# Kernel tuning notes

Measured on AMD Instinct MI355X. Metric: run time of the kernel, lower is better.

## Reference

```python
import jax, jax.numpy as jnp
import numpy as np

B, T, S, DIN, H = 64, 512, 4, 64, 128  # slices S, per-slice input DIN, per-slice hidden H
HTOT = S * H  # 512


def setup_inputs() -> dict:
    key = jax.random.key(0)
    ks = jax.random.split(key, 6)
    stdv = 1.0 / np.sqrt(HTOT)
    u = lambda k, shape: jax.random.uniform(k, shape, jnp.float32, -stdv, stdv)
    x = jax.random.normal(ks[0], (B, T, S * DIN), jnp.float32)
    Ws = u(ks[1], (S, DIN, 4 * H))      # stacked per-slice input weights
    Us = u(ks[2], (S, H, 4 * H))        # stacked per-slice recurrent weights
    biases = u(ks[3], (S, 4 * H))       # stacked per-slice biases
    Wc = u(ks[4], (HTOT, 4 * HTOT))     # connector weights
    bc = u(ks[5], (4 * HTOT,))          # connector biases
    return {"x": x, "Ws": Ws, "Us": Us, "biases": biases, "Wc": Wc, "bc": bc}


def reference(x, Ws, Us, biases, Wc, bc):
    b, t, _ = x.shape
    xt = jnp.swapaxes(x.reshape(b, t, S, DIN), 0, 1)  # (T, B, S, DIN)
    h0 = jnp.zeros((b, HTOT), x.dtype)
    c0 = jnp.zeros((b, HTOT), x.dtype)

    def step(carry, x_t):
        h, c = carry
        hs = h.reshape(b, S, H)
        # block-diagonal per-slice gates: (B, S, 4H)
        gates = (jnp.einsum('bsi,sio->bso', x_t, Ws)
                 + jnp.einsum('bsh,sho->bso', hs, Us)
                 + biases)
        i1 = jax.nn.sigmoid(gates[..., :H]).reshape(b, HTOT)
        f1 = jax.nn.sigmoid(gates[..., H:2 * H]).reshape(b, HTOT)
        g1 = jnp.tanh(gates[..., 2 * H:3 * H]).reshape(b, HTOT)
        o1 = jax.nn.sigmoid(gates[..., 3 * H:]).reshape(b, HTOT)
        # connector stage
        i_t = jax.nn.sigmoid(i1 @ Wc[:, :HTOT] + bc[:HTOT])
        f_t = jax.nn.sigmoid(f1 @ Wc[:, HTOT:2 * HTOT] + bc[HTOT:2 * HTOT])
        g_t = jnp.tanh(g1 @ Wc[:, 2 * HTOT:3 * HTOT] + bc[2 * HTOT:3 * HTOT])
        o_t = jax.nn.sigmoid(o1 @ Wc[:, 3 * HTOT:] + bc[3 * HTOT:])
        c_new = f_t * c + i_t * g_t
        h_new = o_t * jnp.tanh(c_new)
        return (h_new, c_new), h_new

    (h_t, c_t), hseq = jax.lax.scan(step, (h0, c0), xt)
    hidden_seq = jnp.swapaxes(hseq, 0, 1)  # (B, T, HTOT)
    return hidden_seq, h_t, c_t
```

## Files before the change

kernel.cpp:

```cpp
#include <hip/hip_runtime.h>
#include <hip/hip_bf16.h>


typedef unsigned short u16;
typedef unsigned long long u64;
typedef __attribute__((ext_vector_type(8))) short short8;
typedef __attribute__((ext_vector_type(4))) float floatx4;

#define NT 256
#define NBLK 128
#define TSTEPS 512

#define WS_FLAG1 0
#define WS_FLAG2 1024
#define WS_H_HI 2048
#define WS_ZERO_BYTES (WS_H_HI + 65536)
#define WS_ACT_HI (WS_ZERO_BYTES)
#define ACT_PLANE 131072

__device__ __forceinline__ float b2f(u16 u) {
  unsigned v = ((unsigned)u) << 16;
  float f;
  __builtin_memcpy(&f, &v, 4);
  return f;
}
__device__ __forceinline__ u16 f2b(float f) {
  __hip_bfloat16 h = __float2bfloat16(f);
  u16 u;
  __builtin_memcpy(&u, &h, 2);
  return u;
}
__device__ __forceinline__ float sigf(float x) { return 1.0f / (1.0f + __expf(-x)); }
__device__ __forceinline__ float tanhf_fast(float x) { return 2.0f * sigf(2.0f * x) - 1.0f; }
__device__ __forceinline__ short8 ld8(const u16* p) { return *(const short8*)p; }

__device__ __forceinline__ short8 lda_frag(const u16* p) {
  union {
    u64 q[2];
    short8 s;
  } u;
  u.q[0] = __hip_atomic_load((const u64*)p, __ATOMIC_RELAXED, __HIP_MEMORY_SCOPE_AGENT);
  u.q[1] = __hip_atomic_load((const u64*)(p + 4), __ATOMIC_RELAXED, __HIP_MEMORY_SCOPE_AGENT);
  return u.s;
}
__device__ __forceinline__ void sta16(u16* p, u16 v) {
  __hip_atomic_store(p, v, __ATOMIC_RELAXED, __HIP_MEMORY_SCOPE_AGENT);
}

__device__ __forceinline__ void split8v(float4 a, float4 b, short8& hi, short8& lo) {
  float v[8] = {a.x, a.y, a.z, a.w, b.x, b.y, b.z, b.w};
#pragma unroll
  for (int i = 0; i < 8; ++i) {
    u16 h = f2b(v[i]);
    hi[i] = (short)h;
    lo[i] = (short)f2b(v[i] - b2f(h));
  }
}

__device__ __forceinline__ void wait_flags(unsigned* flags, int nmask, unsigned target) {
  if (threadIdx.x < 64) {
    const int fi = threadIdx.x & nmask;
    int spins = 0;
    for (;;) {
      const unsigned v =
          __hip_atomic_load(&flags[fi], __ATOMIC_RELAXED, __HIP_MEMORY_SCOPE_AGENT);
      if (__ballot(v >= target) == ~0ULL) break;
      if (++spins > (1 << 24)) break;
      __builtin_amdgcn_s_sleep(1);
    }
  }
  __syncthreads();
}
__device__ __forceinline__ void arrive_flags(unsigned* flags, int myidx, unsigned target) {
  asm volatile("s_waitcnt vmcnt(0)" ::: "memory");
  __syncthreads();
  if (threadIdx.x == 0)
    __hip_atomic_store(&flags[myidx], target, __ATOMIC_RELAXED, __HIP_MEMORY_SCOPE_AGENT);
}

__global__ void __launch_bounds__(NT) init_ws_kernel(unsigned* w, int n) {
  int i = blockIdx.x * blockDim.x + threadIdx.x;
  const int st = gridDim.x * blockDim.x;
  for (; i < n; i += st) w[i] = 0u;
}

__global__ void __launch_bounds__(NT, 1) slicelstm_kernel(
    const float* __restrict__ x, const float* __restrict__ Ws,
    const float* __restrict__ Us, const float* __restrict__ biases,
    const float* __restrict__ Wc, const float* __restrict__ bcg,
    float* __restrict__ out, u16* __restrict__ act_hi, u16* __restrict__ h_hi,
    unsigned* __restrict__ flagbase) {
  __shared__ __align__(16) u16 W1H[64 * 200];
  __shared__ __align__(16) u16 W2H[64 * 520];
  __shared__ float gx[4][16][17];

  const int tid = threadIdx.x;
  const int blk = blockIdx.x;
  const int q = blk & 3;
  const int jt = blk >> 2;
  const int j0 = jt * 16;
  const int s = j0 >> 7;
  const int jbase = j0 & 127;
  unsigned* flags1 = flagbase + q * 64;
  unsigned* flags2 = flagbase + 256 + (q * 4 + s) * 16;

  for (int i = tid; i < 64 * 192; i += NT) {
    const int r = i / 192, k = i % 192;
    const int col = (r >> 4) * 128 + jbase + (r & 15);
    const float w = (k < 64) ? Ws[(size_t)(s * 64 + k) * 512 + col]
                             : Us[(size_t)(s * 128 + (k - 64)) * 512 + col];
    W1H[r * 200 + k] = f2b(w);
  }
  for (int i = tid; i < 64 * 512; i += NT) {
    const int r = i >> 9, k = i & 511;
    const int col = (r >> 4) * 512 + j0 + (r & 15);
    W2H[r * 520 + k] = f2b(Wc[(size_t)k * 2048 + col]);
  }

  const int lane = tid & 63;
  const int g = tid >> 6;
  const int lm = lane & 15;
  const int lq = lane >> 4;
  const int ko = lq * 8;

  short8 w1l[6], w2l[16];
#pragma unroll
  for (int kt = 0; kt < 6; ++kt) {
    const int col = (g << 7) + jbase + lm;
#pragma unroll
    for (int e = 0; e < 8; ++e) {
      const int k = kt * 32 + ko + e;
      const float w = (k < 64) ? Ws[(size_t)(s * 64 + k) * 512 + col]
                               : Us[(size_t)(s * 128 + (k - 64)) * 512 + col];
      w1l[kt][e] = (short)f2b(w - b2f(f2b(w)));
    }
  }
#pragma unroll
  for (int kt = 0; kt < 16; ++kt) {
    const int col = (g << 9) + j0 + lm;
#pragma unroll
    for (int e = 0; e < 8; ++e) {
      const float w = Wc[(size_t)(kt * 32 + ko + e) * 2048 + col];
      w2l[kt][e] = (short)f2b(w - b2f(f2b(w)));
    }
  }
  const float biasv = biases[s * 512 + (g << 7) + jbase + lm];
  const float bcv = bcg[(g << 9) + j0 + lm];
  __syncthreads();

  const u16* w1r = &W1H[((g << 4) + lm) * 200];
  const u16* w2r = &W2H[((g << 4) + lm) * 520];
  const int brow = q * 16 + lm;
  const float* xrow = x + (size_t)brow * (512 * 256) + s * 64;
  const int hbase = brow * 512 + s * 128;
  const int arow_off = ((g << 6) + brow) * 512;

  const int p3b = tid >> 4, p3j = tid & 15;
  const int p3ci = (q * 16 + p3b) * 512 + j0 + p3j;
  const size_t obase = (size_t)(q * 16 + p3b) * TSTEPS * 512 + j0 + p3j;
  float creg = 0.f, hprev = 0.f;

  float4 xa0, xb0, xa1, xb1;
  {
    const float* xp = xrow;
    xa0 = *(const float4*)(xp + ko);
    xb0 = *(const float4*)(xp + ko + 4);
    xa1 = *(const float4*)(xp + 32 + ko);
    xb1 = *(const float4*)(xp + 32 + ko + 4);
  }

  for (int t = 0; t < TSTEPS; ++t) {
    short8 xh[2], xl[2];
    split8v(xa0, xb0, xh[0], xl[0]);
    split8v(xa1, xb1, xh[1], xl[1]);
    floatx4 accA = {0.f, 0.f, 0.f, 0.f}, accB = {0.f, 0.f, 0.f, 0.f};
    floatx4 accC = {0.f, 0.f, 0.f, 0.f};
#pragma unroll
    for (int kt = 0; kt < 2; ++kt) {
      const short8 bh = ld8(w1r + kt * 32 + ko);
      accA = __builtin_amdgcn_mfma_f32_16x16x32_bf16(xh[kt], bh, accA, 0, 0, 0);
      accB = __builtin_amdgcn_mfma_f32_16x16x32_bf16(xl[kt], bh, accB, 0, 0, 0);
      accC = __builtin_amdgcn_mfma_f32_16x16x32_bf16(xh[kt], w1l[kt], accC, 0, 0, 0);
    }

    wait_flags(flags2, 7, (unsigned)t);

    short8 hh[4];
#pragma unroll
    for (int kt = 0; kt < 4; ++kt) hh[kt] = lda_frag(&h_hi[hbase + kt * 32 + ko]);
    asm volatile("s_waitcnt vmcnt(0)" ::: "memory");
    __builtin_amdgcn_sched_barrier(0);

    {
#pragma unroll
      for (int kt = 0; kt < 4; ++kt) {
        const short8 bh = ld8(w1r + 64 + kt * 32 + ko);
        accA = __builtin_amdgcn_mfma_f32_16x16x32_bf16(hh[kt], bh, accA, 0, 0, 0);
        accC = __builtin_amdgcn_mfma_f32_16x16x32_bf16(hh[kt], w1l[2 + kt], accC, 0, 0, 0);
      }
      const int pp = (t & 1) * ACT_PLANE;
#pragma unroll
      for (int r = 0; r < 4; ++r) {
        const int b = q * 16 + lq * 4 + r;
        const float pre = accA[r] + accB[r] + accC[r] + biasv;
        const float a = (g == 2) ? tanhf_fast(pre) : sigf(pre);
        sta16(&act_hi[pp + ((g << 6) + b) * 512 + j0 + lm], f2b(a));
      }
    }
    arrive_flags(flags1, jt, (unsigned)(t + 1));
    if (t > 0) __builtin_nontemporal_store(hprev, &out[obase + (size_t)(t - 1) * 512]);
    {
      const float* xp = xrow + (size_t)(t < TSTEPS - 1 ? (t + 1) : t) * 256;
      xa0 = *(const float4*)(xp + ko);
      xb0 = *(const float4*)(xp + ko + 4);
      xa1 = *(const float4*)(xp + 32 + ko);
      xb1 = *(const float4*)(xp + 32 + ko + 4);
    }
    __builtin_amdgcn_sched_barrier(0);
    wait_flags(flags1, 31, (unsigned)(t + 1));

    short8 Ah[16];
    {
      const u16* ahp = act_hi + (t & 1) * ACT_PLANE + arow_off;
#pragma unroll
      for (int kt = 0; kt < 16; ++kt) Ah[kt] = lda_frag(ahp + kt * 32 + ko);
    }
    asm volatile("s_waitcnt vmcnt(0)" ::: "memory");
    __builtin_amdgcn_sched_barrier(0);
    floatx4 a2a = {0.f, 0.f, 0.f, 0.f}, a2b = {0.f, 0.f, 0.f, 0.f};
    floatx4 a2c = {0.f, 0.f, 0.f, 0.f}, a2d = {0.f, 0.f, 0.f, 0.f};
#pragma unroll
    for (int kt = 0; kt < 16; kt += 2) {
      const int kb0 = kt * 32 + ko, kb1 = kb0 + 32;
      const short8 Bh0 = ld8(w2r + kb0), Bh1 = ld8(w2r + kb1);
      a2a = __builtin_amdgcn_mfma_f32_16x16x32_bf16(Ah[kt], Bh0, a2a, 0, 0, 0);
      a2b = __builtin_amdgcn_mfma_f32_16x16x32_bf16(Ah[kt], w2l[kt], a2b, 0, 0, 0);
      a2c = __builtin_amdgcn_mfma_f32_16x16x32_bf16(Ah[kt + 1], Bh1, a2c, 0, 0, 0);
      a2d = __builtin_amdgcn_mfma_f32_16x16x32_bf16(Ah[kt + 1], w2l[kt + 1], a2d, 0, 0, 0);
    }
#pragma unroll
    for (int r = 0; r < 4; ++r)
      gx[g][lq * 4 + r][lm] = (a2a[r] + a2c[r]) + (a2b[r] + a2d[r]) + bcv;
    __syncthreads();

    {
      const float it = sigf(gx[0][p3b][p3j]);
      const float ft = sigf(gx[1][p3b][p3j]);
      const float gt = tanhf_fast(gx[2][p3b][p3j]);
      const float ot = sigf(gx[3][p3b][p3j]);
      const float cn = ft * creg + it * gt;
      creg = cn;
      const float h = ot * tanhf_fast(cn);
      hprev = h;
      if (t < TSTEPS - 1) {
        sta16(&h_hi[p3ci], f2b(h));
      } else {
        __builtin_nontemporal_store(h, &out[obase + (size_t)t * 512]);
        __builtin_nontemporal_store(h, &out[16777216 + p3ci]);
        __builtin_nontemporal_store(cn, &out[16777216 + 32768 + p3ci]);
      }
    }
    if (t < TSTEPS - 1) arrive_flags(flags2, jt & 7, (unsigned)(t + 1));
  }
}

extern "C" void kernel_launch(void* const* d_in, const int* in_sizes, int n_in,
                              void* d_out, int out_size, void* d_ws, size_t ws_size,
                              hipStream_t stream) {
  const float* x = (const float*)d_in[0];
  const float* Ws = (const float*)d_in[1];
  const float* Us = (const float*)d_in[2];
  const float* biases = (const float*)d_in[3];
  const float* Wc = (const float*)d_in[4];
  const float* bc = (const float*)d_in[5];

  char* ws = (char*)d_ws;
  unsigned* flagbase = (unsigned*)(ws + WS_FLAG1);
  u16* h_hi = (u16*)(ws + WS_H_HI);
  u16* act_hi = (u16*)(ws + WS_ACT_HI);

  hipLaunchKernelGGL(init_ws_kernel, dim3(64), dim3(NT), 0, stream, (unsigned*)ws,
                     WS_ZERO_BYTES / 4);
  hipLaunchKernelGGL(slicelstm_kernel, dim3(NBLK), dim3(NT), 0, stream, x, Ws, Us,
                     biases, Wc, bc, (float*)d_out, act_hi, h_hi, flagbase);
}
```

Before: 4.442 ms.

## Replace flag barriers with per-element step tags packed beside bf16 data

Removes the separate flag arrays and the wait/arrive barrier protocol. Each bf16 value is now stored in a 32-bit word together with a step tag, and consumers spin-poll the data itself until every tag matches the expected step. The aim is to cut the store-drain, __syncthreads and flag round-trip latency on the critical path of each recurrent step. In exchange the activation and hidden-state traffic doubles, the workspace that must be zeroed grows, and a failed poll re-reads the whole fragment set.

```diff
diff --git a/kernel.cpp b/kernel.cpp
--- a/kernel.cpp
+++ b/kernel.cpp
@@ -11,12 +11,10 @@
 #define NBLK 128
 #define TSTEPS 512
 
-#define WS_FLAG1 0
-#define WS_FLAG2 1024
-#define WS_H_HI 2048
-#define WS_ZERO_BYTES (WS_H_HI + 65536)
-#define WS_ACT_HI (WS_ZERO_BYTES)
-#define ACT_PLANE 131072
+#define WS_H 0
+#define WS_ACT 131072
+#define ACT_PLANE_U32 131072
+#define WS_ZERO_BYTES (131072 + 2 * 524288)
 
 __device__ __forceinline__ float b2f(u16 u) {
   unsigned v = ((unsigned)u) << 16;
@@ -34,16 +32,10 @@
 __device__ __forceinline__ float tanhf_fast(float x) { return 2.0f * sigf(2.0f * x) - 1.0f; }
 __device__ __forceinline__ short8 ld8(const u16* p) { return *(const short8*)p; }
 
-__device__ __forceinline__ short8 lda_frag(const u16* p) {
-  union {
-    u64 q[2];
-    short8 s;
-  } u;
-  u.q[0] = __hip_atomic_load((const u64*)p, __ATOMIC_RELAXED, __HIP_MEMORY_SCOPE_AGENT);
-  u.q[1] = __hip_atomic_load((const u64*)(p + 4), __ATOMIC_RELAXED, __HIP_MEMORY_SCOPE_AGENT);
-  return u.s;
-}
-__device__ __forceinline__ void sta16(u16* p, u16 v) {
+__device__ __forceinline__ u64 ald64(const u64* p) {
+  return __hip_atomic_load(p, __ATOMIC_RELAXED, __HIP_MEMORY_SCOPE_AGENT);
+}
+__device__ __forceinline__ void ast32(unsigned* p, unsigned v) {
   __hip_atomic_store(p, v, __ATOMIC_RELAXED, __HIP_MEMORY_SCOPE_AGENT);
 }
 
@@ -57,26 +49,19 @@
   }
 }
 
-__device__ __forceinline__ void wait_flags(unsigned* flags, int nmask, unsigned target) {
-  if (threadIdx.x < 64) {
-    const int fi = threadIdx.x & nmask;
-    int spins = 0;
-    for (;;) {
-      const unsigned v =
-          __hip_atomic_load(&flags[fi], __ATOMIC_RELAXED, __HIP_MEMORY_SCOPE_AGENT);
-      if (__ballot(v >= target) == ~0ULL) break;
-      if (++spins > (1 << 24)) break;
-      __builtin_amdgcn_s_sleep(1);
-    }
-  }
-  __syncthreads();
-}
-__device__ __forceinline__ void arrive_flags(unsigned* flags, int myidx, unsigned target) {
-  asm volatile("s_waitcnt vmcnt(0)" ::: "memory");
-  __syncthreads();
-  if (threadIdx.x == 0)
-    __hip_atomic_store(&flags[myidx], target, __ATOMIC_RELAXED, __HIP_MEMORY_SCOPE_AGENT);
-}
+#define TAG_MASK 0x0000ffff0000ffffULL
+
+#define EXTRACT4(dst, d0, d1, d2, d3)              \
+  do {                                             \
+    dst[0] = (short)((d0) >> 16);                  \
+    dst[1] = (short)((d0) >> 48);                  \
+    dst[2] = (short)((d1) >> 16);                  \
+    dst[3] = (short)((d1) >> 48);                  \
+    dst[4] = (short)((d2) >> 16);                  \
+    dst[5] = (short)((d2) >> 48);                  \
+    dst[6] = (short)((d3) >> 16);                  \
+    dst[7] = (short)((d3) >> 48);                  \
+  } while (0)
 
 __global__ void __launch_bounds__(NT) init_ws_kernel(unsigned* w, int n) {
   int i = blockIdx.x * blockDim.x + threadIdx.x;
@@ -88,8 +73,8 @@
     const float* __restrict__ x, const float* __restrict__ Ws,
     const float* __restrict__ Us, const float* __restrict__ biases,
     const float* __restrict__ Wc, const float* __restrict__ bcg,
-    float* __restrict__ out, u16* __restrict__ act_hi, u16* __restrict__ h_hi,
-    unsigned* __restrict__ flagbase) {
+    float* __restrict__ out, unsigned* __restrict__ actbuf,
+    unsigned* __restrict__ hbuf) {
   __shared__ __align__(16) u16 W1H[64 * 200];
   __shared__ __align__(16) u16 W2H[64 * 520];
   __shared__ float gx[4][16][17];
@@ -101,8 +86,6 @@
   const int j0 = jt * 16;
   const int s = j0 >> 7;
   const int jbase = j0 & 127;
-  unsigned* flags1 = flagbase + q * 64;
-  unsigned* flags2 = flagbase + 256 + (q * 4 + s) * 16;
 
   for (int i = tid; i < 64 * 192; i += NT) {
     const int r = i / 192, k = i % 192;
@@ -183,13 +166,24 @@
       accC = __builtin_amdgcn_mfma_f32_16x16x32_bf16(xh[kt], w1l[kt], accC, 0, 0, 0);
     }
 
-    wait_flags(flags2, 7, (unsigned)t);
-
     short8 hh[4];
-#pragma unroll
-    for (int kt = 0; kt < 4; ++kt) hh[kt] = lda_frag(&h_hi[hbase + kt * 32 + ko]);
-    asm volatile("s_waitcnt vmcnt(0)" ::: "memory");
-    __builtin_amdgcn_sched_barrier(0);
+    {
+      const u64 tg2 = ((u64)(unsigned)t << 32) | (unsigned)t;
+      int tries = 0;
+      for (;;) {
+        u64 bad = 0;
+#pragma unroll
+        for (int kt = 0; kt < 4; ++kt) {
+          const u64* p = (const u64*)&hbuf[hbase + kt * 32 + ko];
+          const u64 d0 = ald64(p), d1 = ald64(p + 1);
+          const u64 d2 = ald64(p + 2), d3 = ald64(p + 3);
+          bad |= ((d0 ^ tg2) | (d1 ^ tg2) | (d2 ^ tg2) | (d3 ^ tg2)) & TAG_MASK;
+          EXTRACT4(hh[kt], d0, d1, d2, d3);
+        }
+        if (__ballot(bad == 0) == ~0ULL) break;
+        if (++tries > (1 << 12)) break;
+      }
+    }
 
     {
 #pragma unroll
@@ -198,16 +192,37 @@
         accA = __builtin_amdgcn_mfma_f32_16x16x32_bf16(hh[kt], bh, accA, 0, 0, 0);
         accC = __builtin_amdgcn_mfma_f32_16x16x32_bf16(hh[kt], w1l[2 + kt], accC, 0, 0, 0);
       }
-      const int pp = (t & 1) * ACT_PLANE;
+      const int pp = (t & 1) * ACT_PLANE_U32;
 #pragma unroll
       for (int r = 0; r < 4; ++r) {
         const int b = q * 16 + lq * 4 + r;
         const float pre = accA[r] + accB[r] + accC[r] + biasv;
         const float a = (g == 2) ? tanhf_fast(pre) : sigf(pre);
-        sta16(&act_hi[pp + ((g << 6) + b) * 512 + j0 + lm], f2b(a));
-      }
-    }
-    arrive_flags(flags1, jt, (unsigned)(t + 1));
+        ast32(&actbuf[pp + ((g << 6) + b) * 512 + j0 + lm],
+              ((unsigned)f2b(a) << 16) | (unsigned)(t + 1));
+      }
+    }
+
+    short8 Ah[16];
+    {
+      const unsigned* ap = actbuf + (t & 1) * ACT_PLANE_U32 + arow_off;
+      const u64 tg2 = ((u64)(unsigned)(t + 1) << 32) | (unsigned)(t + 1);
+      int tries = 0;
+      for (;;) {
+        u64 bad = 0;
+#pragma unroll
+        for (int kt = 0; kt < 16; ++kt) {
+          const u64* p = (const u64*)(ap + kt * 32 + ko);
+          const u64 d0 = ald64(p), d1 = ald64(p + 1);
+          const u64 d2 = ald64(p + 2), d3 = ald64(p + 3);
+          bad |= ((d0 ^ tg2) | (d1 ^ tg2) | (d2 ^ tg2) | (d3 ^ tg2)) & TAG_MASK;
+          EXTRACT4(Ah[kt], d0, d1, d2, d3);
+        }
+        if (__ballot(bad == 0) == ~0ULL) break;
+        if (++tries > (1 << 12)) break;
+      }
+    }
+
     if (t > 0) __builtin_nontemporal_store(hprev, &out[obase + (size_t)(t - 1) * 512]);
     {
       const float* xp = xrow + (size_t)(t < TSTEPS - 1 ? (t + 1) : t) * 256;
@@ -216,17 +231,7 @@
       xa1 = *(const float4*)(xp + 32 + ko);
       xb1 = *(const float4*)(xp + 32 + ko + 4);
     }
-    __builtin_amdgcn_sched_barrier(0);
-    wait_flags(flags1, 31, (unsigned)(t + 1));
-
-    short8 Ah[16];
-    {
-      const u16* ahp = act_hi + (t & 1) * ACT_PLANE + arow_off;
-#pragma unroll
-      for (int kt = 0; kt < 16; ++kt) Ah[kt] = lda_frag(ahp + kt * 32 + ko);
-    }
-    asm volatile("s_waitcnt vmcnt(0)" ::: "memory");
-    __builtin_amdgcn_sched_barrier(0);
+
     floatx4 a2a = {0.f, 0.f, 0.f, 0.f}, a2b = {0.f, 0.f, 0.f, 0.f};
     floatx4 a2c = {0.f, 0.f, 0.f, 0.f}, a2d = {0.f, 0.f, 0.f, 0.f};
 #pragma unroll
@@ -253,14 +258,14 @@
       const float h = ot * tanhf_fast(cn);
       hprev = h;
       if (t < TSTEPS - 1) {
-        sta16(&h_hi[p3ci], f2b(h));
+        ast32(&hbuf[p3ci], ((unsigned)f2b(h) << 16) | (unsigned)(t + 1));
       } else {
         __builtin_nontemporal_store(h, &out[obase + (size_t)t * 512]);
         __builtin_nontemporal_store(h, &out[16777216 + p3ci]);
         __builtin_nontemporal_store(cn, &out[16777216 + 32768 + p3ci]);
       }
     }
-    if (t < TSTEPS - 1) arrive_flags(flags2, jt & 7, (unsigned)(t + 1));
+    __syncthreads();
   }
 }
 
@@ -275,12 +280,11 @@
   const float* bc = (const float*)d_in[5];
 
   char* ws = (char*)d_ws;
-  unsigned* flagbase = (unsigned*)(ws + WS_FLAG1);
-  u16* h_hi = (u16*)(ws + WS_H_HI);
-  u16* act_hi = (u16*)(ws + WS_ACT_HI);
-
-  hipLaunchKernelGGL(init_ws_kernel, dim3(64), dim3(NT), 0, stream, (unsigned*)ws,
+  unsigned* hbuf = (unsigned*)(ws + WS_H);
+  unsigned* actbuf = (unsigned*)(ws + WS_ACT);
+
+  hipLaunchKernelGGL(init_ws_kernel, dim3(128), dim3(NT), 0, stream, (unsigned*)ws,
                      WS_ZERO_BYTES / 4);
   hipLaunchKernelGGL(slicelstm_kernel, dim3(NBLK), dim3(NT), 0, stream, x, Ws, Us,
-                     biases, Wc, bc, (float*)d_out, act_hi, h_hi, flagbase);
-}
+                     biases, Wc, bc, (float*)d_out, actbuf, hbuf);
+}
```

Result: slower. 9.617 ms (+116.5%).

## Halve grid and interleave two batch groups per block to overlap barrier waits

Applied to the files above, without the earlier changes.

Each block now handles two batch quarters (A and B) instead of one, so the grid shrinks from 128 to 64 blocks. The stage-1 and stage-2 work for the two groups is interleaved, so one group's computation can fill the time spent waiting on the other group's inter-block flags. This is meant to hide cross-block synchronisation latency on the sequential critical path. In exchange each block does twice the serial work per step and needs more registers, which may lengthen the per-step critical path.

```diff
diff --git a/kernel.cpp b/kernel.cpp
--- a/kernel.cpp
+++ b/kernel.cpp
@@ -8,7 +8,7 @@
 typedef __attribute__((ext_vector_type(4))) float floatx4;
 
 #define NT 256
-#define NBLK 128
+#define NBLK 64
 #define TSTEPS 512
 
 #define WS_FLAG1 0
@@ -92,17 +92,20 @@
     unsigned* __restrict__ flagbase) {
   __shared__ __align__(16) u16 W1H[64 * 200];
   __shared__ __align__(16) u16 W2H[64 * 520];
-  __shared__ float gx[4][16][17];
+  __shared__ float gx[2][4][16][17];
 
   const int tid = threadIdx.x;
   const int blk = blockIdx.x;
-  const int q = blk & 3;
-  const int jt = blk >> 2;
+  const int qA = blk & 1;
+  const int qB = qA + 2;
+  const int jt = blk >> 1;
   const int j0 = jt * 16;
   const int s = j0 >> 7;
   const int jbase = j0 & 127;
-  unsigned* flags1 = flagbase + q * 64;
-  unsigned* flags2 = flagbase + 256 + (q * 4 + s) * 16;
+  unsigned* flags1A = flagbase + qA * 64;
+  unsigned* flags1B = flagbase + qB * 64;
+  unsigned* flags2A = flagbase + 256 + (qA * 4 + s) * 16;
+  unsigned* flags2B = flagbase + 256 + (qB * 4 + s) * 16;
 
   for (int i = tid; i < 64 * 192; i += NT) {
     const int r = i / 192, k = i % 192;
@@ -150,117 +153,208 @@
 
   const u16* w1r = &W1H[((g << 4) + lm) * 200];
   const u16* w2r = &W2H[((g << 4) + lm) * 520];
-  const int brow = q * 16 + lm;
-  const float* xrow = x + (size_t)brow * (512 * 256) + s * 64;
-  const int hbase = brow * 512 + s * 128;
-  const int arow_off = ((g << 6) + brow) * 512;
+  const int browA = qA * 16 + lm;
+  const int browB = qB * 16 + lm;
+  const float* xrowA = x + (size_t)browA * (512 * 256) + s * 64;
+  const float* xrowB = x + (size_t)browB * (512 * 256) + s * 64;
+  const int hbaseA = browA * 512 + s * 128;
+  const int hbaseB = browB * 512 + s * 128;
+  const int arowA = ((g << 6) + browA) * 512;
+  const int arowB = ((g << 6) + browB) * 512;
 
   const int p3b = tid >> 4, p3j = tid & 15;
-  const int p3ci = (q * 16 + p3b) * 512 + j0 + p3j;
-  const size_t obase = (size_t)(q * 16 + p3b) * TSTEPS * 512 + j0 + p3j;
-  float creg = 0.f, hprev = 0.f;
-
-  float4 xa0, xb0, xa1, xb1;
+  const int p3ciA = (qA * 16 + p3b) * 512 + j0 + p3j;
+  const int p3ciB = (qB * 16 + p3b) * 512 + j0 + p3j;
+  const size_t obaseA = (size_t)(qA * 16 + p3b) * TSTEPS * 512 + j0 + p3j;
+  const size_t obaseB = (size_t)(qB * 16 + p3b) * TSTEPS * 512 + j0 + p3j;
+  float cregA = 0.f, hprevA = 0.f, cregB = 0.f, hprevB = 0.f;
+
+  float4 xa0A, xb0A, xa1A, xb1A, xa0B, xb0B, xa1B, xb1B;
   {
-    const float* xp = xrow;
-    xa0 = *(const float4*)(xp + ko);
-    xb0 = *(const float4*)(xp + ko + 4);
-    xa1 = *(const float4*)(xp + 32 + ko);
-    xb1 = *(const float4*)(xp + 32 + ko + 4);
+    const float* xp = xrowA;
+    xa0A = *(const float4*)(xp + ko);
+    xb0A = *(const float4*)(xp + ko + 4);
+    xa1A = *(const float4*)(xp + 32 + ko);
+    xb1A = *(const float4*)(xp + 32 + ko + 4);
+    const float* xq = xrowB;
+    xa0B = *(const float4*)(xq + ko);
+    xb0B = *(const float4*)(xq + ko + 4);
+    xa1B = *(const float4*)(xq + 32 + ko);
+    xb1B = *(const float4*)(xq + 32 + ko + 4);
   }
 
   for (int t = 0; t < TSTEPS; ++t) {
-    short8 xh[2], xl[2];
-    split8v(xa0, xb0, xh[0], xl[0]);
-    split8v(xa1, xb1, xh[1], xl[1]);
-    floatx4 accA = {0.f, 0.f, 0.f, 0.f}, accB = {0.f, 0.f, 0.f, 0.f};
-    floatx4 accC = {0.f, 0.f, 0.f, 0.f};
+    const int pp = (t & 1) * ACT_PLANE;
+    floatx4 aA = {0.f, 0.f, 0.f, 0.f}, aB = {0.f, 0.f, 0.f, 0.f};
+    floatx4 aC = {0.f, 0.f, 0.f, 0.f};
+    {
+      short8 xh[2], xl[2];
+      split8v(xa0A, xb0A, xh[0], xl[0]);
+      split8v(xa1A, xb1A, xh[1], xl[1]);
+#pragma unroll
+      for (int kt = 0; kt < 2; ++kt) {
+        const short8 bh = ld8(w1r + kt * 32 + ko);
+        aA = __builtin_amdgcn_mfma_f32_16x16x32_bf16(xh[kt], bh, aA, 0, 0, 0);
+        aB = __builtin_amdgcn_mfma_f32_16x16x32_bf16(xl[kt], bh, aB, 0, 0, 0);
+        aC = __builtin_amdgcn_mfma_f32_16x16x32_bf16(xh[kt], w1l[kt], aC, 0, 0, 0);
+      }
+      wait_flags(flags2A, 7, (unsigned)t);
+      short8 hh[4];
+#pragma unroll
+      for (int kt = 0; kt < 4; ++kt) hh[kt] = lda_frag(&h_hi[hbaseA + kt * 32 + ko]);
+      asm volatile("s_waitcnt vmcnt(0)" ::: "memory");
+      __builtin_amdgcn_sched_barrier(0);
+#pragma unroll
+      for (int kt = 0; kt < 4; ++kt) {
+        const short8 bh = ld8(w1r + 64 + kt * 32 + ko);
+        aA = __builtin_amdgcn_mfma_f32_16x16x32_bf16(hh[kt], bh, aA, 0, 0, 0);
+        aC = __builtin_amdgcn_mfma_f32_16x16x32_bf16(hh[kt], w1l[2 + kt], aC, 0, 0, 0);
+      }
+#pragma unroll
+      for (int r = 0; r < 4; ++r) {
+        const int b = qA * 16 + lq * 4 + r;
+        const float pre = aA[r] + aB[r] + aC[r] + biasv;
+        const float a = (g == 2) ? tanhf_fast(pre) : sigf(pre);
+        sta16(&act_hi[pp + ((g << 6) + b) * 512 + j0 + lm], f2b(a));
+      }
+    }
+    floatx4 bA = {0.f, 0.f, 0.f, 0.f}, bB = {0.f, 0.f, 0.f, 0.f};
+    floatx4 bC = {0.f, 0.f, 0.f, 0.f};
+    short8 xhB[2], xlB[2];
+    split8v(xa0B, xb0B, xhB[0], xlB[0]);
+    split8v(xa1B, xb1B, xhB[1], xlB[1]);
 #pragma unroll
     for (int kt = 0; kt < 2; ++kt) {
       const short8 bh = ld8(w1r + kt * 32 + ko);
-      accA = __builtin_amdgcn_mfma_f32_16x16x32_bf16(xh[kt], bh, accA, 0, 0, 0);
-      accB = __builtin_amdgcn_mfma_f32_16x16x32_bf16(xl[kt], bh, accB, 0, 0, 0);
-      accC = __builtin_amdgcn_mfma_f32_16x16x32_bf16(xh[kt], w1l[kt], accC, 0, 0, 0);
-    }
-
-    wait_flags(flags2, 7, (unsigned)t);
-
-    short8 hh[4];
-#pragma unroll
-    for (int kt = 0; kt < 4; ++kt) hh[kt] = lda_frag(&h_hi[hbase + kt * 32 + ko]);
-    asm volatile("s_waitcnt vmcnt(0)" ::: "memory");
-    __builtin_amdgcn_sched_barrier(0);
-
-    {
+      bA = __builtin_amdgcn_mfma_f32_16x16x32_bf16(xhB[kt], bh, bA, 0, 0, 0);
+      bB = __builtin_amdgcn_mfma_f32_16x16x32_bf16(xlB[kt], bh, bB, 0, 0, 0);
+      bC = __builtin_amdgcn_mfma_f32_16x16x32_bf16(xhB[kt], w1l[kt], bC, 0, 0, 0);
+    }
+    arrive_flags(flags1A, jt, (unsigned)(t + 1));
+    if (t > 0) __builtin_nontemporal_store(hprevA, &out[obaseA + (size_t)(t - 1) * 512]);
+    {
+      const float* xp = xrowA + (size_t)(t < TSTEPS - 1 ? (t + 1) : t) * 256;
+      xa0A = *(const float4*)(xp + ko);
+      xb0A = *(const float4*)(xp + ko + 4);
+      xa1A = *(const float4*)(xp + 32 + ko);
+      xb1A = *(const float4*)(xp + 32 + ko + 4);
+    }
+    {
+      wait_flags(flags2B, 7, (unsigned)t);
+      short8 hh[4];
+#pragma unroll
+      for (int kt = 0; kt < 4; ++kt) hh[kt] = lda_frag(&h_hi[hbaseB + kt * 32 + ko]);
+      asm volatile("s_waitcnt vmcnt(0)" ::: "memory");
+      __builtin_amdgcn_sched_barrier(0);
 #pragma unroll
       for (int kt = 0; kt < 4; ++kt) {
         const short8 bh = ld8(w1r + 64 + kt * 32 + ko);
-        accA = __builtin_amdgcn_mfma_f32_16x16x32_bf16(hh[kt], bh, accA, 0, 0, 0);
-        accC = __builtin_amdgcn_mfma_f32_16x16x32_bf16(hh[kt], w1l[2 + kt], accC, 0, 0, 0);
-      }
-      const int pp = (t & 1) * ACT_PLANE;
+        bA = __builtin_amdgcn_mfma_f32_16x16x32_bf16(hh[kt], bh, bA, 0, 0, 0);
+        bC = __builtin_amdgcn_mfma_f32_16x16x32_bf16(hh[kt], w1l[2 + kt], bC, 0, 0, 0);
+      }
 #pragma unroll
       for (int r = 0; r < 4; ++r) {
-        const int b = q * 16 + lq * 4 + r;
-        const float pre = accA[r] + accB[r] + accC[r] + biasv;
+        const int b = qB * 16 + lq * 4 + r;
+        const float pre = bA[r] + bB[r] + bC[r] + biasv;
         const float a = (g == 2) ? tanhf_fast(pre) : sigf(pre);
         sta16(&act_hi[pp + ((g << 6) + b) * 512 + j0 + lm], f2b(a));
       }
     }
-    arrive_flags(flags1, jt, (unsigned)(t + 1));
-    if (t > 0) __builtin_nontemporal_store(hprev, &out[obase + (size_t)(t - 1) * 512]);
-    {
-      const float* xp = xrow + (size_t)(t < TSTEPS - 1 ? (t + 1) : t) * 256;
-      xa0 = *(const float4*)(xp + ko);
-      xb0 = *(const float4*)(xp + ko + 4);
-      xa1 = *(const float4*)(xp + 32 + ko);
-      xb1 = *(const float4*)(xp + 32 + ko + 4);
-    }
-    __builtin_amdgcn_sched_barrier(0);
-    wait_flags(flags1, 31, (unsigned)(t + 1));
-
-    short8 Ah[16];
-    {
-      const u16* ahp = act_hi + (t & 1) * ACT_PLANE + arow_off;
+    arrive_flags(flags1B, jt, (unsigned)(t + 1));
+    if (t > 0) __builtin_nontemporal_store(hprevB, &out[obaseB + (size_t)(t - 1) * 512]);
+    {
+      const float* xp = xrowB + (size_t)(t < TSTEPS - 1 ? (t + 1) : t) * 256;
+      xa0B = *(const float4*)(xp + ko);
+      xb0B = *(const float4*)(xp + ko + 4);
+      xa1B = *(const float4*)(xp + 32 + ko);
+      xb1B = *(const float4*)(xp + 32 + ko + 4);
+    }
+
+    {
+      wait_flags(flags1A, 31, (unsigned)(t + 1));
+      short8 Ah[16];
+      const u16* ahp = act_hi + pp + arowA;
 #pragma unroll
       for (int kt = 0; kt < 16; ++kt) Ah[kt] = lda_frag(ahp + kt * 32 + ko);
-    }
-    asm volatile("s_waitcnt vmcnt(0)" ::: "memory");
-    __builtin_amdgcn_sched_barrier(0);
-    floatx4 a2a = {0.f, 0.f, 0.f, 0.f}, a2b = {0.f, 0.f, 0.f, 0.f};
-    floatx4 a2c = {0.f, 0.f, 0.f, 0.f}, a2d = {0.f, 0.f, 0.f, 0.f};
-#pragma unroll
-    for (int kt = 0; kt < 16; kt += 2) {
-      const int kb0 = kt * 32 + ko, kb1 = kb0 + 32;
-      const short8 Bh0 = ld8(w2r + kb0), Bh1 = ld8(w2r + kb1);
-      a2a = __builtin_amdgcn_mfma_f32_16x16x32_bf16(Ah[kt], Bh0, a2a, 0, 0, 0);
-      a2b = __builtin_amdgcn_mfma_f32_16x16x32_bf16(Ah[kt], w2l[kt], a2b, 0, 0, 0);
-      a2c = __builtin_amdgcn_mfma_f32_16x16x32_bf16(Ah[kt + 1], Bh1, a2c, 0, 0, 0);
-      a2d = __builtin_amdgcn_mfma_f32_16x16x32_bf16(Ah[kt + 1], w2l[kt + 1], a2d, 0, 0, 0);
-    }
-#pragma unroll
-    for (int r = 0; r < 4; ++r)
-      gx[g][lq * 4 + r][lm] = (a2a[r] + a2c[r]) + (a2b[r] + a2d[r]) + bcv;
+      asm volatile("s_waitcnt vmcnt(0)" ::: "memory");
+      __builtin_amdgcn_sched_barrier(0);
+      floatx4 c0 = {0.f, 0.f, 0.f, 0.f}, c1 = {0.f, 0.f, 0.f, 0.f};
+      floatx4 c2 = {0.f, 0.f, 0.f, 0.f}, c3 = {0.f, 0.f, 0.f, 0.f};
+#pragma unroll
+      for (int kt = 0; kt < 16; kt += 2) {
+        const int kb0 = kt * 32 + ko, kb1 = kb0 + 32;
+        const short8 Bh0 = ld8(w2r + kb0), Bh1 = ld8(w2r + kb1);
+        c0 = __builtin_amdgcn_mfma_f32_16x16x32_bf16(Ah[kt], Bh0, c0, 0, 0, 0);
+        c1 = __builtin_amdgcn_mfma_f32_16x16x32_bf16(Ah[kt], w2l[kt], c1, 0, 0, 0);
+        c2 = __builtin_amdgcn_mfma_f32_16x16x32_bf16(Ah[kt + 1], Bh1, c2, 0, 0, 0);
+        c3 = __builtin_amdgcn_mfma_f32_16x16x32_bf16(Ah[kt + 1], w2l[kt + 1], c3, 0, 0, 0);
+      }
+#pragma unroll
+      for (int r = 0; r < 4; ++r)
+        gx[0][g][lq * 4 + r][lm] = (c0[r] + c2[r]) + (c1[r] + c3[r]) + bcv;
+    }
     __syncthreads();
-
-    {
-      const float it = sigf(gx[0][p3b][p3j]);
-      const float ft = sigf(gx[1][p3b][p3j]);
-      const float gt = tanhf_fast(gx[2][p3b][p3j]);
-      const float ot = sigf(gx[3][p3b][p3j]);
-      const float cn = ft * creg + it * gt;
-      creg = cn;
+    {
+      const float it = sigf(gx[0][0][p3b][p3j]);
+      const float ft = sigf(gx[0][1][p3b][p3j]);
+      const float gt = tanhf_fast(gx[0][2][p3b][p3j]);
+      const float ot = sigf(gx[0][3][p3b][p3j]);
+      const float cn = ft * cregA + it * gt;
+      cregA = cn;
       const float h = ot * tanhf_fast(cn);
-      hprev = h;
+      hprevA = h;
       if (t < TSTEPS - 1) {
-        sta16(&h_hi[p3ci], f2b(h));
+        sta16(&h_hi[p3ciA], f2b(h));
       } else {
-        __builtin_nontemporal_store(h, &out[obase + (size_t)t * 512]);
-        __builtin_nontemporal_store(h, &out[16777216 + p3ci]);
-        __builtin_nontemporal_store(cn, &out[16777216 + 32768 + p3ci]);
-      }
-    }
-    if (t < TSTEPS - 1) arrive_flags(flags2, jt & 7, (unsigned)(t + 1));
+        __builtin_nontemporal_store(h, &out[obaseA + (size_t)t * 512]);
+        __builtin_nontemporal_store(h, &out[16777216 + p3ciA]);
+        __builtin_nontemporal_store(cregA, &out[16777216 + 32768 + p3ciA]);
+      }
+    }
+    if (t < TSTEPS - 1) arrive_flags(flags2A, jt & 7, (unsigned)(t + 1));
+
+    {
+      wait_flags(flags1B, 31, (unsigned)(t + 1));
+      short8 Ah[16];
+      const u16* ahp = act_hi + pp + arowB;
+#pragma unroll
+      for (int kt = 0; kt < 16; ++kt) Ah[kt] = lda_frag(ahp + kt * 32 + ko);
+      asm volatile("s_waitcnt vmcnt(0)" ::: "memory");
+      __builtin_amdgcn_sched_barrier(0);
+      floatx4 c0 = {0.f, 0.f, 0.f, 0.f}, c1 = {0.f, 0.f, 0.f, 0.f};
+      floatx4 c2 = {0.f, 0.f, 0.f, 0.f}, c3 = {0.f, 0.f, 0.f, 0.f};
+#pragma unroll
+      for (int kt = 0; kt < 16; kt += 2) {
+        const int kb0 = kt * 32 + ko, kb1 = kb0 + 32;
+        const short8 Bh0 = ld8(w2r + kb0), Bh1 = ld8(w2r + kb1);
+        c0 = __builtin_amdgcn_mfma_f32_16x16x32_bf16(Ah[kt], Bh0, c0, 0, 0, 0);
+        c1 = __builtin_amdgcn_mfma_f32_16x16x32_bf16(Ah[kt], w2l[kt], c1, 0, 0, 0);
+        c2 = __builtin_amdgcn_mfma_f32_16x16x32_bf16(Ah[kt + 1], Bh1, c2, 0, 0, 0);
+        c3 = __builtin_amdgcn_mfma_f32_16x16x32_bf16(Ah[kt + 1], w2l[kt + 1], c3, 0, 0, 0);
+      }
+#pragma unroll
+      for (int r = 0; r < 4; ++r)
+        gx[1][g][lq * 4 + r][lm] = (c0[r] + c2[r]) + (c1[r] + c3[r]) + bcv;
+    }
+    __syncthreads();
+    {
+      const float it = sigf(gx[1][0][p3b][p3j]);
+      const float ft = sigf(gx[1][1][p3b][p3j]);
+      const float gt = tanhf_fast(gx[1][2][p3b][p3j]);
+      const float ot = sigf(gx[1][3][p3b][p3j]);
+      const float cn = ft * cregB + it * gt;
+      cregB = cn;
+      const float h = ot * tanhf_fast(cn);
+      hprevB = h;
+      if (t < TSTEPS - 1) {
+        sta16(&h_hi[p3ciB], f2b(h));
+      } else {
+        __builtin_nontemporal_store(h, &out[obaseB + (size_t)t * 512]);
+        __builtin_nontemporal_store(h, &out[16777216 + p3ciB]);
+        __builtin_nontemporal_store(cregB, &out[16777216 + 32768 + p3ciB]);
+      }
+    }
+    if (t < TSTEPS - 1) arrive_flags(flags2B, jt & 7, (unsigned)(t + 1));
   }
 }
 
```

After: 8.268 ms. +86.1%, slower.

## Replace h-state flag barrier with step-tagged h values polled directly

Applied to the files above, without the earlier changes.

The per-step flags2 barrier guarding the hidden state is removed. Each h value is now stored as a 32-bit word that packs the bf16 value with the timestep tag, and readers spin-load their h fragments until every tag matches the current step. This is meant to remove the arrive/wait round trip (waitcnt, syncthreads, flag store, flag poll) on the critical recurrent path, and it issues the h loads early. In exchange the h buffer doubles in size, each load carries more bytes, and readers must re-poll the data itself rather than a small flag array.

```diff
diff --git a/kernel.cpp b/kernel.cpp
--- a/kernel.cpp
+++ b/kernel.cpp
@@ -12,9 +12,8 @@
 #define TSTEPS 512
 
 #define WS_FLAG1 0
-#define WS_FLAG2 1024
-#define WS_H_HI 2048
-#define WS_ZERO_BYTES (WS_H_HI + 65536)
+#define WS_H 1024
+#define WS_ZERO_BYTES (WS_H + 131072)
 #define WS_ACT_HI (WS_ZERO_BYTES)
 #define ACT_PLANE 131072
 
@@ -46,6 +45,12 @@
 __device__ __forceinline__ void sta16(u16* p, u16 v) {
   __hip_atomic_store(p, v, __ATOMIC_RELAXED, __HIP_MEMORY_SCOPE_AGENT);
 }
+__device__ __forceinline__ u64 ald64(const u64* p) {
+  return __hip_atomic_load(p, __ATOMIC_RELAXED, __HIP_MEMORY_SCOPE_AGENT);
+}
+__device__ __forceinline__ void ast32(unsigned* p, unsigned v) {
+  __hip_atomic_store(p, v, __ATOMIC_RELAXED, __HIP_MEMORY_SCOPE_AGENT);
+}
 
 __device__ __forceinline__ void split8v(float4 a, float4 b, short8& hi, short8& lo) {
   float v[8] = {a.x, a.y, a.z, a.w, b.x, b.y, b.z, b.w};
@@ -56,6 +61,19 @@
     lo[i] = (short)f2b(v[i] - b2f(h));
   }
 }
+
+#define TAG_MASK 0x0000ffff0000ffffULL
+#define EXTRACT4(dst, d0, d1, d2, d3) \
+  do {                                \
+    dst[0] = (short)((d0) >> 16);     \
+    dst[1] = (short)((d0) >> 48);     \
+    dst[2] = (short)((d1) >> 16);     \
+    dst[3] = (short)((d1) >> 48);     \
+    dst[4] = (short)((d2) >> 16);     \
+    dst[5] = (short)((d2) >> 48);     \
+    dst[6] = (short)((d3) >> 16);     \
+    dst[7] = (short)((d3) >> 48);     \
+  } while (0)
 
 __device__ __forceinline__ void wait_flags(unsigned* flags, int nmask, unsigned target) {
   if (threadIdx.x < 64) {
@@ -88,7 +106,7 @@
     const float* __restrict__ x, const float* __restrict__ Ws,
     const float* __restrict__ Us, const float* __restrict__ biases,
     const float* __restrict__ Wc, const float* __restrict__ bcg,
-    float* __restrict__ out, u16* __restrict__ act_hi, u16* __restrict__ h_hi,
+    float* __restrict__ out, u16* __restrict__ act_hi, unsigned* __restrict__ hbuf,
     unsigned* __restrict__ flagbase) {
   __shared__ __align__(16) u16 W1H[64 * 200];
   __shared__ __align__(16) u16 W2H[64 * 520];
@@ -102,7 +120,6 @@
   const int s = j0 >> 7;
   const int jbase = j0 & 127;
   unsigned* flags1 = flagbase + q * 64;
-  unsigned* flags2 = flagbase + 256 + (q * 4 + s) * 16;
 
   for (int i = tid; i < 64 * 192; i += NT) {
     const int r = i / 192, k = i % 192;
@@ -170,6 +187,14 @@
   }
 
   for (int t = 0; t < TSTEPS; ++t) {
+    u64 hd[4][4];
+#pragma unroll
+    for (int kt = 0; kt < 4; ++kt) {
+      const u64* p = (const u64*)&hbuf[hbase + kt * 32 + ko];
+#pragma unroll
+      for (int i = 0; i < 4; ++i) hd[kt][i] = ald64(p + i);
+    }
+
     short8 xh[2], xl[2];
     split8v(xa0, xb0, xh[0], xl[0]);
     split8v(xa1, xb1, xh[1], xl[1]);
@@ -183,13 +208,29 @@
       accC = __builtin_amdgcn_mfma_f32_16x16x32_bf16(xh[kt], w1l[kt], accC, 0, 0, 0);
     }
 
-    wait_flags(flags2, 7, (unsigned)t);
-
     short8 hh[4];
-#pragma unroll
-    for (int kt = 0; kt < 4; ++kt) hh[kt] = lda_frag(&h_hi[hbase + kt * 32 + ko]);
-    asm volatile("s_waitcnt vmcnt(0)" ::: "memory");
-    __builtin_amdgcn_sched_barrier(0);
+    {
+      const u64 tg2 = ((u64)(unsigned)t << 32) | (unsigned)t;
+      int tries = 0;
+      for (;;) {
+        u64 bad = 0;
+#pragma unroll
+        for (int kt = 0; kt < 4; ++kt) {
+          bad |= ((hd[kt][0] ^ tg2) | (hd[kt][1] ^ tg2) | (hd[kt][2] ^ tg2) |
+                  (hd[kt][3] ^ tg2)) &
+                 TAG_MASK;
+          EXTRACT4(hh[kt], hd[kt][0], hd[kt][1], hd[kt][2], hd[kt][3]);
+        }
+        if (__ballot(bad == 0) == ~0ULL) break;
+        if (++tries > (1 << 12)) break;
+#pragma unroll
+        for (int kt = 0; kt < 4; ++kt) {
+          const u64* p = (const u64*)&hbuf[hbase + kt * 32 + ko];
+#pragma unroll
+          for (int i = 0; i < 4; ++i) hd[kt][i] = ald64(p + i);
+        }
+      }
+    }
 
     {
 #pragma unroll
@@ -253,14 +294,13 @@
       const float h = ot * tanhf_fast(cn);
       hprev = h;
       if (t < TSTEPS - 1) {
-        sta16(&h_hi[p3ci], f2b(h));
+        ast32(&hbuf[p3ci], ((unsigned)f2b(h) << 16) | (unsigned)(t + 1));
       } else {
         __builtin_nontemporal_store(h, &out[obase + (size_t)t * 512]);
         __builtin_nontemporal_store(h, &out[16777216 + p3ci]);
         __builtin_nontemporal_store(cn, &out[16777216 + 32768 + p3ci]);
       }
     }
-    if (t < TSTEPS - 1) arrive_flags(flags2, jt & 7, (unsigned)(t + 1));
   }
 }
 
@@ -276,11 +316,11 @@
 
   char* ws = (char*)d_ws;
   unsigned* flagbase = (unsigned*)(ws + WS_FLAG1);
-  u16* h_hi = (u16*)(ws + WS_H_HI);
+  unsigned* hbuf = (unsigned*)(ws + WS_H);
   u16* act_hi = (u16*)(ws + WS_ACT_HI);
 
   hipLaunchKernelGGL(init_ws_kernel, dim3(64), dim3(NT), 0, stream, (unsigned*)ws,
                      WS_ZERO_BYTES / 4);
   hipLaunchKernelGGL(slicelstm_kernel, dim3(NBLK), dim3(NT), 0, stream, x, Ws, Us,
-                     biases, Wc, bc, (float*)d_out, act_hi, h_hi, flagbase);
-}
+                     biases, Wc, bc, (float*)d_out, act_hi, hbuf, flagbase);
+}
```

Result: slower. 5.669 ms (+27.6%).
